# Performance work log

Measured on AMD Instinct MI355X. Metric: run time of the kernel, lower is better.

## Reference

```python
import jax, jax.numpy as jnp
import numpy as np

N = 20000       # nodes
E = 320000      # edges (avg in-degree 16)
IN_DIM = 128
HID = 64
HEADS = 4
NUM_GRAPHS = 128
N_CLASSES = 10


def setup_inputs() -> dict:
    key = jax.random.key(0)
    ks = jax.random.split(key, 8)
    h = jax.random.normal(ks[0], (N, IN_DIM), jnp.float32)
    src = jax.random.randint(ks[1], (E,), 0, N)
    dst = jax.random.randint(ks[2], (E,), 0, N)
    graph_ids = jnp.sort(jax.random.randint(ks[3], (N,), 0, NUM_GRAPHS))
    # DotGatConv fc weights (no bias in DGL DotGatConv), classifier Linear w/ bias
    W1 = jax.random.normal(ks[4], (IN_DIM, HID * HEADS), jnp.float32) / np.sqrt(IN_DIM).astype(np.float32)
    W2 = jax.random.normal(ks[5], (HID * HEADS, HID), jnp.float32) / np.sqrt(HID * HEADS).astype(np.float32)
    Wc = jax.random.normal(ks[6], (HID, N_CLASSES), jnp.float32) / np.sqrt(HID).astype(np.float32)
    bc = jnp.zeros((N_CLASSES,), jnp.float32)
    return {"h": h, "src": src, "dst": dst, "graph_ids": graph_ids,
            "W1": W1, "W2": W2, "Wc": Wc, "bc": bc}


def dot_gat(x, src, dst, W, num_heads):
    """DGL DotGatConv: scaled dot-product attention over graph edges."""
    n = x.shape[0]
    d = W.shape[1] // num_heads
    ft = (x @ W).reshape(n, num_heads, d)          # [N,H,D]
    hs = ft[src]                                    # [E,H,D] source feats
    hd = ft[dst]                                    # [E,H,D] dest feats
    e = (hs * hd).sum(-1) / jnp.sqrt(jnp.float32(d))  # [E,H] edge scores
    # edge softmax over incoming edges per destination node (stable)
    m = jax.ops.segment_max(e, dst, num_segments=n)    # [N,H]
    ee = jnp.exp(e - m[dst])                           # [E,H]
    den = jax.ops.segment_sum(ee, dst, num_segments=n)[dst]  # [E,H]
    a = ee / den
    # aggregate attention-weighted source messages at destination
    return jax.ops.segment_sum(hs * a[..., None], dst, num_segments=n)  # [N,H,D]


def reference(h, src, dst, graph_ids, W1, W2, Wc, bc):
    n = h.shape[0]
    x = jax.nn.relu(dot_gat(h, src, dst, W1, HEADS)).reshape(n, -1)   # [N, HID*HEADS]
    x = jax.nn.relu(dot_gat(x, src, dst, W2, 1)).reshape(n, -1)       # [N, HID]
    # AvgPooling: mean of node features per graph
    cnt = jax.ops.segment_sum(jnp.ones((n,), x.dtype), graph_ids, num_segments=NUM_GRAPHS)
    pooled = jax.ops.segment_sum(x, graph_ids, num_segments=NUM_GRAPHS) / jnp.maximum(cnt, 1.0)[:, None]
    return pooled @ Wc + bc                                            # [NUM_GRAPHS, N_CLASSES]
```

## Files before the change

### kernel.cpp

```cpp
#include <hip/hip_runtime.h>
#include <hip/hip_bf16.h>

typedef __attribute__((ext_vector_type(8))) __bf16 bf16x8;
typedef __attribute__((ext_vector_type(8))) unsigned short ushort8;
typedef __attribute__((ext_vector_type(4))) float floatx4;

#define N_NODES   20000
#define N_EDGES   320000
#define IN_DIM    128
#define HID       64
#define HEADS     4
#define NUM_GRAPHS 128
#define N_CLASSES 10
#define BCAP      128

__device__ inline float cvt_load(const void* p, int i, int isb) {
    return isb ? __bfloat162float(((const __hip_bfloat16*)p)[i]) : ((const float*)p)[i];
}

__device__ inline unsigned short bf16bits(float v) {
    return __builtin_bit_cast(unsigned short, __float2bfloat16(v));
}

__device__ inline unsigned pack2(float a, float b) {
    return (unsigned)bf16bits(a) | ((unsigned)bf16bits(b) << 16);
}

__device__ inline floatx4 unpack4(uint2 u) {
    floatx4 f;
    f.x = __uint_as_float(u.x << 16);
    f.y = __uint_as_float(u.x & 0xffff0000u);
    f.z = __uint_as_float(u.y << 16);
    f.w = __uint_as_float(u.y & 0xffff0000u);
    return f;
}

__global__ void prep_kernel(const void* W1, const void* W2, const void* Wc, const void* bc,
                            unsigned short* W1t, unsigned short* W2t, float* Wcf, float* bcf,
                            const int* __restrict__ src, const int* __restrict__ dst,
                            int* __restrict__ cnt, int* __restrict__ bucket,
                            const unsigned int* __restrict__ hw, int* flag) {
    int b = blockIdx.x;
    const int n1 = IN_DIM * HID * HEADS;
    const int n2 = HID * HEADS * HID;
    const int n3 = HID * N_CLASSES;
    const int n4 = N_CLASSES;
    if (b < 195) {
        __shared__ int s_bad;
        if (threadIdx.x == 0) s_bad = 0;
        __syncthreads();
        int bad = 0;
        for (int i = threadIdx.x; i < 4096; i += 256) {
            float v = __uint_as_float(hw[i]);
            if (!(fabsf(v) <= 1e20f)) bad = 1;
        }
        if (bad) atomicOr(&s_bad, 1);
        __syncthreads();
        int isb = s_bad;
        if (b == 0 && threadIdx.x == 0) *flag = isb;

        int i = b * 256 + threadIdx.x;
        if (i < n1) {
            int k = i >> 8, n = i & 255;
            W1t[n * 128 + k] = bf16bits(cvt_load(W1, i, isb));
        } else if (i < n1 + n2) {
            int j = i - n1;
            int k = j >> 6, n = j & 63;
            W2t[n * 256 + k] = bf16bits(cvt_load(W2, j, isb));
        } else if (i < n1 + n2 + n3) {
            int j = i - n1 - n2;
            Wcf[j] = cvt_load(Wc, j, isb);
        } else if (i < n1 + n2 + n3 + n4) {
            int j = i - n1 - n2 - n3;
            bcf[j] = cvt_load(bc, j, isb);
        }
    } else {
        int e = (b - 195) * 256 + threadIdx.x;
        if (e < N_EDGES) {
            int d = dst[e];
            int pos = atomicAdd(&cnt[d], 1);
            if (pos < BCAP) bucket[d * BCAP + pos] = src[e];
        }
    }
}

__global__ __launch_bounds__(256) void gemm1_kernel(const void* __restrict__ h_any,
                                                    const unsigned short* __restrict__ Bt,
                                                    unsigned short* __restrict__ C, int M,
                                                    const int* flag) {
    int wave = threadIdx.x >> 6;
    int lane = threadIdx.x & 63;
    int q = lane >> 4, r = lane & 15;
    int m0 = blockIdx.x * 64;
    int n0 = wave * 64;
    floatx4 acc[4][4] = {};
    bf16x8 bfrag[4][4];
#pragma unroll
    for (int ni = 0; ni < 4; ++ni)
#pragma unroll
        for (int kk = 0; kk < 4; ++kk)
            bfrag[ni][kk] = *(const bf16x8*)(Bt + (n0 + ni * 16 + r) * 128 + kk * 32 + q * 8);
    if (*flag) {
        const unsigned short* A = (const unsigned short*)h_any;
#pragma unroll
        for (int kk = 0; kk < 4; ++kk) {
            bf16x8 afrag[4];
#pragma unroll
            for (int mi = 0; mi < 4; ++mi) {
                int row = m0 + mi * 16 + r;
                bf16x8 a = {};
                if (row < M) a = *(const bf16x8*)(A + row * 128 + kk * 32 + q * 8);
                afrag[mi] = a;
            }
#pragma unroll
            for (int mi = 0; mi < 4; ++mi)
#pragma unroll
                for (int ni = 0; ni < 4; ++ni)
                    acc[mi][ni] = __builtin_amdgcn_mfma_f32_16x16x32_bf16(afrag[mi], bfrag[ni][kk], acc[mi][ni], 0, 0, 0);
        }
    } else {
        const float* A = (const float*)h_any;
#pragma unroll
        for (int kk = 0; kk < 4; ++kk) {
            bf16x8 afrag[4];
#pragma unroll
            for (int mi = 0; mi < 4; ++mi) {
                int row = m0 + mi * 16 + r;
                bf16x8 a = {};
                if (row < M) {
                    const floatx4* p = (const floatx4*)(A + row * 128 + kk * 32 + q * 8);
                    floatx4 f0 = p[0], f1 = p[1];
                    ushort8 u;
                    u[0] = bf16bits(f0.x); u[1] = bf16bits(f0.y);
                    u[2] = bf16bits(f0.z); u[3] = bf16bits(f0.w);
                    u[4] = bf16bits(f1.x); u[5] = bf16bits(f1.y);
                    u[6] = bf16bits(f1.z); u[7] = bf16bits(f1.w);
                    a = __builtin_bit_cast(bf16x8, u);
                }
                afrag[mi] = a;
            }
#pragma unroll
            for (int mi = 0; mi < 4; ++mi)
#pragma unroll
                for (int ni = 0; ni < 4; ++ni)
                    acc[mi][ni] = __builtin_amdgcn_mfma_f32_16x16x32_bf16(afrag[mi], bfrag[ni][kk], acc[mi][ni], 0, 0, 0);
        }
    }
#pragma unroll
    for (int mi = 0; mi < 4; ++mi)
#pragma unroll
        for (int rr = 0; rr < 4; ++rr) {
            int row = m0 + mi * 16 + q * 4 + rr;
            if (row < M) {
#pragma unroll
                for (int ni = 0; ni < 4; ++ni)
                    C[row * 256 + n0 + ni * 16 + r] = bf16bits(acc[mi][ni][rr]);
            }
        }
}

__global__ __launch_bounds__(512) void attn4proj_kernel(const unsigned short* __restrict__ ft,
                                                        const int* __restrict__ cnt,
                                                        const int* __restrict__ bucket,
                                                        const unsigned short* __restrict__ W2t,
                                                        unsigned short* __restrict__ ft2) {
    __shared__ unsigned short x1t[8][256];
    int w    = threadIdx.x >> 6;
    int lane = threadIdx.x & 63;
    int dstv = blockIdx.x * 8 + w;
    floatx4 hd = unpack4(*(const uint2*)(ft + dstv * 256 + lane * 4));
    int deg  = min(cnt[dstv], BCAP);
    int base = dstv * BCAP;
    float l = 0.f;
    floatx4 acc = {0.f, 0.f, 0.f, 0.f};
    int i0 = 0;
    for (; i0 + 4 <= deg; i0 += 4) {
        int sn0 = bucket[base + i0],     sn1 = bucket[base + i0 + 1];
        int sn2 = bucket[base + i0 + 2], sn3 = bucket[base + i0 + 3];
        uint2 r0 = *(const uint2*)(ft + sn0 * 256 + lane * 4);
        uint2 r1 = *(const uint2*)(ft + sn1 * 256 + lane * 4);
        uint2 r2 = *(const uint2*)(ft + sn2 * 256 + lane * 4);
        uint2 r3 = *(const uint2*)(ft + sn3 * 256 + lane * 4);
        floatx4 h0 = unpack4(r0), h1 = unpack4(r1), h2 = unpack4(r2), h3 = unpack4(r3);
        float p0 = h0.x * hd.x + h0.y * hd.y + h0.z * hd.z + h0.w * hd.w;
        float p1 = h1.x * hd.x + h1.y * hd.y + h1.z * hd.z + h1.w * hd.w;
        float p2 = h2.x * hd.x + h2.y * hd.y + h2.z * hd.z + h2.w * hd.w;
        float p3 = h3.x * hd.x + h3.y * hd.y + h3.z * hd.z + h3.w * hd.w;
        p0 += __shfl_xor(p0, 1); p1 += __shfl_xor(p1, 1); p2 += __shfl_xor(p2, 1); p3 += __shfl_xor(p3, 1);
        p0 += __shfl_xor(p0, 2); p1 += __shfl_xor(p1, 2); p2 += __shfl_xor(p2, 2); p3 += __shfl_xor(p3, 2);
        p0 += __shfl_xor(p0, 4); p1 += __shfl_xor(p1, 4); p2 += __shfl_xor(p2, 4); p3 += __shfl_xor(p3, 4);
        p0 += __shfl_xor(p0, 8); p1 += __shfl_xor(p1, 8); p2 += __shfl_xor(p2, 8); p3 += __shfl_xor(p3, 8);
        float w0 = __expf(p0 * 0.125f);
        float w1 = __expf(p1 * 0.125f);
        float w2 = __expf(p2 * 0.125f);
        float w3 = __expf(p3 * 0.125f);
        l += (w0 + w1) + (w2 + w3);
        acc.x += w0 * h0.x + w1 * h1.x + w2 * h2.x + w3 * h3.x;
        acc.y += w0 * h0.y + w1 * h1.y + w2 * h2.y + w3 * h3.y;
        acc.z += w0 * h0.z + w1 * h1.z + w2 * h2.z + w3 * h3.z;
        acc.w += w0 * h0.w + w1 * h1.w + w2 * h2.w + w3 * h3.w;
    }
    for (; i0 < deg; ++i0) {
        int sn = bucket[base + i0];
        floatx4 hs = unpack4(*(const uint2*)(ft + sn * 256 + lane * 4));
        float p = hs.x * hd.x + hs.y * hd.y + hs.z * hd.z + hs.w * hd.w;
        p += __shfl_xor(p, 1); p += __shfl_xor(p, 2);
        p += __shfl_xor(p, 4); p += __shfl_xor(p, 8);
        float wgt = __expf(p * 0.125f);
        l += wgt;
        acc.x += wgt * hs.x; acc.y += wgt * hs.y;
        acc.z += wgt * hs.z; acc.w += wgt * hs.w;
    }
    float inv = (l > 0.f) ? 1.f / l : 0.f;
    unsigned* xr = (unsigned*)&x1t[w][lane * 4];
    xr[0] = pack2(fmaxf(acc.x * inv, 0.f), fmaxf(acc.y * inv, 0.f));
    xr[1] = pack2(fmaxf(acc.z * inv, 0.f), fmaxf(acc.w * inv, 0.f));
    __syncthreads();
    if (w < 4) {
        int q = lane >> 4, r = lane & 15;
        floatx4 pacc = {0.f, 0.f, 0.f, 0.f};
#pragma unroll
        for (int kk = 0; kk < 8; ++kk) {
            bf16x8 bfrag = *(const bf16x8*)(W2t + (w * 16 + r) * 256 + kk * 32 + q * 8);
            bf16x8 afrag = {};
            if (r < 8) afrag = *(const bf16x8*)(&x1t[r][kk * 32 + q * 8]);
            pacc = __builtin_amdgcn_mfma_f32_16x16x32_bf16(afrag, bfrag, pacc, 0, 0, 0);
        }
#pragma unroll
        for (int rr = 0; rr < 4; ++rr) {
            int row = q * 4 + rr;
            if (row < 8)
                ft2[(blockIdx.x * 8 + row) * 64 + w * 16 + r] = bf16bits(pacc[rr]);
        }
    }
}

__global__ __launch_bounds__(256) void attn_h1_kernel(const unsigned short* __restrict__ ft,
                                                      const int* __restrict__ cnt,
                                                      const int* __restrict__ bucket,
                                                      float* __restrict__ out) {
    int dstv = blockIdx.x * 4 + (threadIdx.x >> 6);
    int lane = threadIdx.x & 63;
    int g = lane >> 4, s = lane & 15;
    int hbase = s * 4;
    floatx4 hd = unpack4(*(const uint2*)(ft + dstv * 64 + hbase));
    int deg  = min(cnt[dstv], BCAP);
    int base = dstv * BCAP;
    float l = 0.f;
    floatx4 acc = {0.f, 0.f, 0.f, 0.f};
    int i0 = 0;
    for (; i0 + 8 <= deg; i0 += 8) {
        int ia = i0 + g, ib = i0 + 4 + g;
        int sa = bucket[base + ia], sb = bucket[base + ib];
        uint2 ra = *(const uint2*)(ft + sa * 64 + hbase);
        uint2 rb = *(const uint2*)(ft + sb * 64 + hbase);
        floatx4 ha = unpack4(ra), hb = unpack4(rb);
        float pa = ha.x * hd.x + ha.y * hd.y + ha.z * hd.z + ha.w * hd.w;
        float pb = hb.x * hd.x + hb.y * hd.y + hb.z * hd.z + hb.w * hd.w;
        pa += __shfl_xor(pa, 1); pb += __shfl_xor(pb, 1);
        pa += __shfl_xor(pa, 2); pb += __shfl_xor(pb, 2);
        pa += __shfl_xor(pa, 4); pb += __shfl_xor(pb, 4);
        pa += __shfl_xor(pa, 8); pb += __shfl_xor(pb, 8);
        float wa = __expf(pa * 0.125f);
        float wb = __expf(pb * 0.125f);
        l += wa + wb;
        acc.x += wa * ha.x + wb * hb.x;
        acc.y += wa * ha.y + wb * hb.y;
        acc.z += wa * ha.z + wb * hb.z;
        acc.w += wa * ha.w + wb * hb.w;
    }
    for (; i0 < deg; i0 += 4) {
        int i = i0 + g;
        bool valid = (i < deg);
        int sn = valid ? bucket[base + i] : 0;
        floatx4 hs = unpack4(*(const uint2*)(ft + sn * 64 + hbase));
        float p = hs.x * hd.x + hs.y * hd.y + hs.z * hd.z + hs.w * hd.w;
        p += __shfl_xor(p, 1); p += __shfl_xor(p, 2);
        p += __shfl_xor(p, 4); p += __shfl_xor(p, 8);
        float wgt = valid ? __expf(p * 0.125f) : 0.f;
        l += wgt;
        acc.x += wgt * hs.x; acc.y += wgt * hs.y;
        acc.z += wgt * hs.z; acc.w += wgt * hs.w;
    }
    l += __shfl_xor(l, 16); l += __shfl_xor(l, 32);
    acc.x += __shfl_xor(acc.x, 16); acc.x += __shfl_xor(acc.x, 32);
    acc.y += __shfl_xor(acc.y, 16); acc.y += __shfl_xor(acc.y, 32);
    acc.z += __shfl_xor(acc.z, 16); acc.z += __shfl_xor(acc.z, 32);
    acc.w += __shfl_xor(acc.w, 16); acc.w += __shfl_xor(acc.w, 32);
    float inv = (l > 0.f) ? 1.f / l : 0.f;
    if (g == 0) {
        floatx4 o = {fmaxf(acc.x * inv, 0.f), fmaxf(acc.y * inv, 0.f),
                     fmaxf(acc.z * inv, 0.f), fmaxf(acc.w * inv, 0.f)};
        *(floatx4*)(out + dstv * 64 + hbase) = o;
    }
}

__global__ __launch_bounds__(256) void poolclass_kernel(const float* __restrict__ x,
                                                        const int* __restrict__ gid,
                                                        const float* __restrict__ Wc,
                                                        const float* __restrict__ bc,
                                                        void* out, const int* flag) {
    __shared__ int s_lo, s_hi;
    __shared__ float part[4][64];
    int g = blockIdx.x;
    int tid = threadIdx.x;
    if (tid == 0) {
        int lo = 0, hi = N_NODES;
        while (lo < hi) { int m = (lo + hi) >> 1; if (gid[m] < g) lo = m + 1; else hi = m; }
        s_lo = lo;
        int lo2 = lo, hi2 = N_NODES;
        while (lo2 < hi2) { int m = (lo2 + hi2) >> 1; if (gid[m] < g + 1) lo2 = m + 1; else hi2 = m; }
        s_hi = lo2;
    }
    __syncthreads();
    int lo = s_lo, hi = s_hi;
    int d = tid & 63, w = tid >> 6;
    float sum = 0.f;
    for (int n = lo + w; n < hi; n += 4) sum += x[n * 64 + d];
    part[w][d] = sum;
    __syncthreads();
    if (w == 0) {
        float tot = part[0][d] + part[1][d] + part[2][d] + part[3][d];
        int cntg = hi - lo;
        float mean = (cntg > 0) ? tot / (float)cntg : 0.f;
        for (int cls = 0; cls < N_CLASSES; ++cls) {
            float p = mean * Wc[d * N_CLASSES + cls];
#pragma unroll
            for (int o = 1; o < 64; o <<= 1) p += __shfl_xor(p, o);
            if (d == 0) {
                float r = p + bc[cls];
                if (*flag) ((__hip_bfloat16*)out)[g * N_CLASSES + cls] = __float2bfloat16(r);
                else       ((float*)out)[g * N_CLASSES + cls] = r;
            }
        }
    }
}

static inline size_t align256(size_t x) { return (x + 255) & ~size_t(255); }

extern "C" void kernel_launch(void* const* d_in, const int* in_sizes, int n_in,
                              void* d_out, int out_size, void* d_ws, size_t ws_size,
                              hipStream_t stream) {
    const void* h_raw  = d_in[0];
    const int*  src    = (const int*)d_in[1];
    const int*  dst    = (const int*)d_in[2];
    const int*  gid    = (const int*)d_in[3];
    const void* W1_raw = d_in[4];
    const void* W2_raw = d_in[5];
    const void* Wc_raw = d_in[6];
    const void* bc_raw = d_in[7];

    char* w = (char*)d_ws;
    int*  flag     = (int*)w;                      w += 256;
    int*  cnt      = (int*)w;                      w += align256(N_NODES * 4);
    int*  bucket   = (int*)w;                      w += align256((size_t)N_NODES * BCAP * 4);
    unsigned short* W1t = (unsigned short*)w;      w += align256(256 * 128 * 2);
    unsigned short* W2t = (unsigned short*)w;      w += align256(64 * 256 * 2);
    float* Wcf     = (float*)w;                    w += align256(HID * N_CLASSES * 4);
    float* bcf     = (float*)w;                    w += 256;
    unsigned short* ft1  = (unsigned short*)w;     w += align256((size_t)N_NODES * 256 * 2);
    unsigned short* ft2  = (unsigned short*)w;     w += align256((size_t)N_NODES * HID * 2);
    float* x2      = (float*)w;                    w += align256((size_t)N_NODES * HID * 4);

    hipMemsetAsync(cnt, 0, N_NODES * sizeof(int), stream);

    hipLaunchKernelGGL(prep_kernel, dim3(195 + 1250), dim3(256), 0, stream,
                       W1_raw, W2_raw, Wc_raw, bc_raw, W1t, W2t, Wcf, bcf,
                       src, dst, cnt, bucket,
                       (const unsigned int*)h_raw, flag);

    hipLaunchKernelGGL(gemm1_kernel, dim3((N_NODES + 63) / 64), dim3(256), 0, stream,
                       h_raw, W1t, ft1, N_NODES, flag);

    hipLaunchKernelGGL(attn4proj_kernel, dim3(N_NODES / 8), dim3(512), 0, stream,
                       ft1, cnt, bucket, W2t, ft2);

    hipLaunchKernelGGL(attn_h1_kernel, dim3(N_NODES / 4), dim3(256), 0, stream,
                       ft2, cnt, bucket, x2);

    hipLaunchKernelGGL(poolclass_kernel, dim3(NUM_GRAPHS), dim3(256), 0, stream,
                       x2, gid, Wcf, bcf, d_out, flag);
}
```

Before: 175.7 us.

## Fuse layer-1 GEMM into prep kernel, reading W1 directly without transpose

Merges the first projection GEMM into the prep kernel as extra blocks, so weight conversion, edge bucketing and the h@W1 GEMM run concurrently in one launch. The W1 transpose buffer goes away: each GEMM block reads W1 straight from its original layout with strided scalar loads and converts it itself, and it redoes the bf16 input detection locally. This saves one kernel launch and the serialization between prep and GEMM. In exchange, every GEMM block makes redundant, uncoalesced loads of W1.

```diff
diff --git a/kernel.cpp b/kernel.cpp
--- a/kernel.cpp
+++ b/kernel.cpp
@@ -14,6 +14,10 @@
 #define N_CLASSES 10
 #define BCAP      128
 
+#define NB_CONV   67
+#define NB_FILL   1250
+#define NB_GEMM1  313
+
 __device__ inline float cvt_load(const void* p, int i, int isb) {
     return isb ? __bfloat162float(((const __hip_bfloat16*)p)[i]) : ((const float*)p)[i];
 }
@@ -35,107 +39,102 @@
     return f;
 }
 
-__global__ void prep_kernel(const void* W1, const void* W2, const void* Wc, const void* bc,
-                            unsigned short* W1t, unsigned short* W2t, float* Wcf, float* bcf,
-                            const int* __restrict__ src, const int* __restrict__ dst,
-                            int* __restrict__ cnt, int* __restrict__ bucket,
-                            const unsigned int* __restrict__ hw, int* flag) {
+__device__ inline int detect_bf16(const unsigned int* hw) {
+    __shared__ int s_bad;
+    if (threadIdx.x == 0) s_bad = 0;
+    __syncthreads();
+    int bad = 0;
+    for (int i = threadIdx.x; i < 4096; i += 256) {
+        float v = __uint_as_float(hw[i]);
+        if (!(fabsf(v) <= 1e20f)) bad = 1;
+    }
+    if (bad) atomicOr(&s_bad, 1);
+    __syncthreads();
+    return s_bad;
+}
+
+__global__ __launch_bounds__(256) void prep_kernel(const void* W1, const void* W2,
+                                                   const void* Wc, const void* bc,
+                                                   unsigned short* W2t, float* Wcf, float* bcf,
+                                                   const int* __restrict__ src,
+                                                   const int* __restrict__ dst,
+                                                   int* __restrict__ cnt, int* __restrict__ bucket,
+                                                   const void* __restrict__ h_any,
+                                                   unsigned short* __restrict__ ft1,
+                                                   int* flag) {
     int b = blockIdx.x;
-    const int n1 = IN_DIM * HID * HEADS;
     const int n2 = HID * HEADS * HID;
     const int n3 = HID * N_CLASSES;
     const int n4 = N_CLASSES;
-    if (b < 195) {
-        __shared__ int s_bad;
-        if (threadIdx.x == 0) s_bad = 0;
-        __syncthreads();
-        int bad = 0;
-        for (int i = threadIdx.x; i < 4096; i += 256) {
-            float v = __uint_as_float(hw[i]);
-            if (!(fabsf(v) <= 1e20f)) bad = 1;
-        }
-        if (bad) atomicOr(&s_bad, 1);
-        __syncthreads();
-        int isb = s_bad;
+    if (b < NB_CONV) {
+        int isb = detect_bf16((const unsigned int*)h_any);
         if (b == 0 && threadIdx.x == 0) *flag = isb;
-
         int i = b * 256 + threadIdx.x;
-        if (i < n1) {
-            int k = i >> 8, n = i & 255;
-            W1t[n * 128 + k] = bf16bits(cvt_load(W1, i, isb));
-        } else if (i < n1 + n2) {
-            int j = i - n1;
-            int k = j >> 6, n = j & 63;
-            W2t[n * 256 + k] = bf16bits(cvt_load(W2, j, isb));
-        } else if (i < n1 + n2 + n3) {
-            int j = i - n1 - n2;
+        if (i < n2) {
+            int k = i >> 6, n = i & 63;
+            W2t[n * 256 + k] = bf16bits(cvt_load(W2, i, isb));
+        } else if (i < n2 + n3) {
+            int j = i - n2;
             Wcf[j] = cvt_load(Wc, j, isb);
-        } else if (i < n1 + n2 + n3 + n4) {
-            int j = i - n1 - n2 - n3;
+        } else if (i < n2 + n3 + n4) {
+            int j = i - n2 - n3;
             bcf[j] = cvt_load(bc, j, isb);
         }
-    } else {
-        int e = (b - 195) * 256 + threadIdx.x;
+    } else if (b < NB_CONV + NB_FILL) {
+        int e = (b - NB_CONV) * 256 + threadIdx.x;
         if (e < N_EDGES) {
             int d = dst[e];
             int pos = atomicAdd(&cnt[d], 1);
             if (pos < BCAP) bucket[d * BCAP + pos] = src[e];
         }
-    }
-}
-
-__global__ __launch_bounds__(256) void gemm1_kernel(const void* __restrict__ h_any,
-                                                    const unsigned short* __restrict__ Bt,
-                                                    unsigned short* __restrict__ C, int M,
-                                                    const int* flag) {
-    int wave = threadIdx.x >> 6;
-    int lane = threadIdx.x & 63;
-    int q = lane >> 4, r = lane & 15;
-    int m0 = blockIdx.x * 64;
-    int n0 = wave * 64;
-    floatx4 acc[4][4] = {};
-    bf16x8 bfrag[4][4];
-#pragma unroll
-    for (int ni = 0; ni < 4; ++ni)
-#pragma unroll
-        for (int kk = 0; kk < 4; ++kk)
-            bfrag[ni][kk] = *(const bf16x8*)(Bt + (n0 + ni * 16 + r) * 128 + kk * 32 + q * 8);
-    if (*flag) {
-        const unsigned short* A = (const unsigned short*)h_any;
+    } else {
+        int b2 = b - (NB_CONV + NB_FILL);
+        int isb = detect_bf16((const unsigned int*)h_any);
+        int wave = threadIdx.x >> 6;
+        int lane = threadIdx.x & 63;
+        int q = lane >> 4, r = lane & 15;
+        int m0 = b2 * 64;
+        int n0 = wave * 64;
+        floatx4 acc[4][4] = {};
+        const unsigned short* W1b = (const unsigned short*)W1;
+        const float*          W1f = (const float*)W1;
+        const unsigned short* Ab  = (const unsigned short*)h_any;
+        const float*          Af  = (const float*)h_any;
 #pragma unroll
         for (int kk = 0; kk < 4; ++kk) {
+            bf16x8 bfrag[4];
+#pragma unroll
+            for (int ni = 0; ni < 4; ++ni) {
+                int n = n0 + ni * 16 + r;
+                int k0 = kk * 32 + q * 8;
+                ushort8 u;
+                if (isb) {
+#pragma unroll
+                    for (int j = 0; j < 8; ++j) u[j] = W1b[(k0 + j) * 256 + n];
+                } else {
+#pragma unroll
+                    for (int j = 0; j < 8; ++j) u[j] = bf16bits(W1f[(k0 + j) * 256 + n]);
+                }
+                bfrag[ni] = __builtin_bit_cast(bf16x8, u);
+            }
             bf16x8 afrag[4];
 #pragma unroll
             for (int mi = 0; mi < 4; ++mi) {
                 int row = m0 + mi * 16 + r;
                 bf16x8 a = {};
-                if (row < M) a = *(const bf16x8*)(A + row * 128 + kk * 32 + q * 8);
-                afrag[mi] = a;
-            }
-#pragma unroll
-            for (int mi = 0; mi < 4; ++mi)
-#pragma unroll
-                for (int ni = 0; ni < 4; ++ni)
-                    acc[mi][ni] = __builtin_amdgcn_mfma_f32_16x16x32_bf16(afrag[mi], bfrag[ni][kk], acc[mi][ni], 0, 0, 0);
-        }
-    } else {
-        const float* A = (const float*)h_any;
-#pragma unroll
-        for (int kk = 0; kk < 4; ++kk) {
-            bf16x8 afrag[4];
-#pragma unroll
-            for (int mi = 0; mi < 4; ++mi) {
-                int row = m0 + mi * 16 + r;
-                bf16x8 a = {};
-                if (row < M) {
-                    const floatx4* p = (const floatx4*)(A + row * 128 + kk * 32 + q * 8);
-                    floatx4 f0 = p[0], f1 = p[1];
-                    ushort8 u;
-                    u[0] = bf16bits(f0.x); u[1] = bf16bits(f0.y);
-                    u[2] = bf16bits(f0.z); u[3] = bf16bits(f0.w);
-                    u[4] = bf16bits(f1.x); u[5] = bf16bits(f1.y);
-                    u[6] = bf16bits(f1.z); u[7] = bf16bits(f1.w);
-                    a = __builtin_bit_cast(bf16x8, u);
+                if (row < N_NODES) {
+                    if (isb) {
+                        a = *(const bf16x8*)(Ab + row * 128 + kk * 32 + q * 8);
+                    } else {
+                        const floatx4* p = (const floatx4*)(Af + row * 128 + kk * 32 + q * 8);
+                        floatx4 f0 = p[0], f1 = p[1];
+                        ushort8 u;
+                        u[0] = bf16bits(f0.x); u[1] = bf16bits(f0.y);
+                        u[2] = bf16bits(f0.z); u[3] = bf16bits(f0.w);
+                        u[4] = bf16bits(f1.x); u[5] = bf16bits(f1.y);
+                        u[6] = bf16bits(f1.z); u[7] = bf16bits(f1.w);
+                        a = __builtin_bit_cast(bf16x8, u);
+                    }
                 }
                 afrag[mi] = a;
             }
@@ -143,20 +142,20 @@
             for (int mi = 0; mi < 4; ++mi)
 #pragma unroll
                 for (int ni = 0; ni < 4; ++ni)
-                    acc[mi][ni] = __builtin_amdgcn_mfma_f32_16x16x32_bf16(afrag[mi], bfrag[ni][kk], acc[mi][ni], 0, 0, 0);
-        }
-    }
-#pragma unroll
-    for (int mi = 0; mi < 4; ++mi)
-#pragma unroll
-        for (int rr = 0; rr < 4; ++rr) {
-            int row = m0 + mi * 16 + q * 4 + rr;
-            if (row < M) {
-#pragma unroll
-                for (int ni = 0; ni < 4; ++ni)
-                    C[row * 256 + n0 + ni * 16 + r] = bf16bits(acc[mi][ni][rr]);
+                    acc[mi][ni] = __builtin_amdgcn_mfma_f32_16x16x32_bf16(afrag[mi], bfrag[ni], acc[mi][ni], 0, 0, 0);
+        }
+#pragma unroll
+        for (int mi = 0; mi < 4; ++mi)
+#pragma unroll
+            for (int rr = 0; rr < 4; ++rr) {
+                int row = m0 + mi * 16 + q * 4 + rr;
+                if (row < N_NODES) {
+#pragma unroll
+                    for (int ni = 0; ni < 4; ++ni)
+                        ft1[row * 256 + n0 + ni * 16 + r] = bf16bits(acc[mi][ni][rr]);
+                }
             }
-        }
+    }
 }
 
 __global__ __launch_bounds__(512) void attn4proj_kernel(const unsigned short* __restrict__ ft,
@@ -354,7 +353,6 @@
     int*  flag     = (int*)w;                      w += 256;
     int*  cnt      = (int*)w;                      w += align256(N_NODES * 4);
     int*  bucket   = (int*)w;                      w += align256((size_t)N_NODES * BCAP * 4);
-    unsigned short* W1t = (unsigned short*)w;      w += align256(256 * 128 * 2);
     unsigned short* W2t = (unsigned short*)w;      w += align256(64 * 256 * 2);
     float* Wcf     = (float*)w;                    w += align256(HID * N_CLASSES * 4);
     float* bcf     = (float*)w;                    w += 256;
@@ -364,13 +362,10 @@
 
     hipMemsetAsync(cnt, 0, N_NODES * sizeof(int), stream);
 
-    hipLaunchKernelGGL(prep_kernel, dim3(195 + 1250), dim3(256), 0, stream,
-                       W1_raw, W2_raw, Wc_raw, bc_raw, W1t, W2t, Wcf, bcf,
+    hipLaunchKernelGGL(prep_kernel, dim3(NB_CONV + NB_FILL + NB_GEMM1), dim3(256), 0, stream,
+                       W1_raw, W2_raw, Wc_raw, bc_raw, W2t, Wcf, bcf,
                        src, dst, cnt, bucket,
-                       (const unsigned int*)h_raw, flag);
-
-    hipLaunchKernelGGL(gemm1_kernel, dim3((N_NODES + 63) / 64), dim3(256), 0, stream,
-                       h_raw, W1t, ft1, N_NODES, flag);
+                       h_raw, ft1, flag);
 
     hipLaunchKernelGGL(attn4proj_kernel, dim3(N_NODES / 8), dim3(512), 0, stream,
                        ft1, cnt, bucket, W2t, ft2);
```

Result: no change. 177.2 us (+0.8%).
